# Optimization experiments

Measured on AMD Instinct MI355X. Metric: run time of the kernel, lower is better.

The kernel has to match this reference:

```python
import jax, jax.numpy as jnp
import numpy as np

B, L, U, G, H = 64, 110, 768, 512, 256
WP = WF = 10
NSP = 2
R = 2 * NSP * NSP      # 8 relation types
NB = 30                # RGCN num_bases
FF = 2048              # torch TransformerEncoderLayer default dim_feedforward
TAG = 7
N = B * L
NEG = -1e9


def _build_edges():
    # static windowed edge structure (all dialogues have length L)
    js, ks = [], []
    for j in range(L):
        for k in range(max(0, j - WP), min(L - 1, j + WF) + 1):
            js.append(j); ks.append(k)
    j = np.asarray(js, np.int32); k = np.asarray(ks, np.int32)
    c = (j >= k).astype(np.int32)  # edge_type suffix: '0' if j<k else '1'
    off = (np.arange(B, dtype=np.int32) * L)[:, None]
    src = (j[None, :] + off).reshape(-1)
    dst = (k[None, :] + off).reshape(-1)
    return src, dst, np.tile(k, B), np.tile(c, B)


def _ln(x, g, b):
    m = x.mean(-1, keepdims=True)
    v = ((x - m) ** 2).mean(-1, keepdims=True)
    return (x - m) / jnp.sqrt(v + 1e-5) * g + b


def _core(x, in_proj_w, in_proj_b, out_proj_w, out_proj_b, ln1_g, ln1_b,
          ff1_w, ff1_b, ff2_w, ff2_b, ln2_g, ln2_b, to_w, to_b, att_w,
          rgcn_basis, rgcn_comp, rgcn_root, rgcn_bias,
          gc_rel_w, gc_rel_b, gc_root_w, clf1_w, clf1_b, clf2_w, clf2_b,
          speaker, src, dst, k_local, cflag):
    # --- SeqContext: 1-layer, 1-head post-norm transformer (eval mode) ---
    qkv = x @ in_proj_w.T + in_proj_b
    q, kk, v = jnp.split(qkv, 3, axis=-1)
    attn = jax.nn.softmax(jnp.einsum('bqd,bkd->bqk', q, kk) / jnp.sqrt(jnp.float32(U)), -1)
    a = jnp.einsum('bqk,bkd->bqd', attn, v) @ out_proj_w.T + out_proj_b
    h = _ln(x + a, ln1_g, ln1_b)
    ff = jax.nn.relu(h @ ff1_w.T + ff1_b) @ ff2_w.T + ff2_b
    h = _ln(h + ff, ln2_g, ln2_b)
    feats = h @ to_w.T + to_b                      # (B, L, G) node features

    # --- EdgeAtt: windowed softmax attention, score[j,k] = x_j^T W x_k ---
    scores = jnp.einsum('bjd,de,bke->bjk', feats, att_w, feats)
    rel = jnp.arange(L)[None, :] - jnp.arange(L)[:, None]
    mask = (rel >= -WP) & (rel <= WF)
    alpha = jax.nn.softmax(jnp.where(mask[None], scores, NEG), -1)  # (B, L, L)

    xf = feats.reshape(N, G)
    edge_norm = alpha.reshape(N, L)[src, k_local]   # alpha[b, j, k] per edge

    # --- edge types from speakers: idx = (s1*NSP + s2)*2 + c ---
    sp = speaker.reshape(N)
    etype = (sp[src] * NSP + sp[dst]) * 2 + cflag

    # --- RGCNConv: basis decomposition, per-(node, relation) mean + root ---
    w_rel = jnp.einsum('rb,bgh->rgh', rgcn_comp, rgcn_basis)   # (R, G, H)
    xproj = jnp.einsum('ng,rgh->rnh', xf, w_rel)               # (R, N, H)
    msg = xproj[etype, src]                                    # (E, H)
    seg = dst * R + etype
    cnt = jax.ops.segment_sum(jnp.ones_like(edge_norm), seg, num_segments=N * R)
    msg = msg / jnp.maximum(cnt[seg], 1.0)[:, None]
    h1 = jax.ops.segment_sum(msg, dst, num_segments=N) + xf @ rgcn_root + rgcn_bias

    # --- GraphConv: sum-aggregate edge-weighted neighbors + root ---
    agg = jax.ops.segment_sum(edge_norm[:, None] * h1[src], dst, num_segments=N)
    h2 = agg @ gc_rel_w.T + gc_rel_b + h1 @ gc_root_w.T

    # --- Classifier (dropout inactive in eval) ---
    z = jnp.concatenate([xf, h2], axis=-1)
    return jax.nn.relu(z @ clf1_w.T + clf1_b) @ clf2_w.T + clf2_b  # (N, TAG)


def setup_inputs():
    key = jax.random.key(0)
    ks = jax.random.split(key, 16)
    def rn(i, shape, scale=0.02):
        return jax.random.normal(ks[i], shape, jnp.float32) * scale
    src, dst, k_local, cflag = _build_edges()
    return {
        'x': jax.random.normal(ks[0], (B, L, U), jnp.float32),
        'in_proj_w': rn(1, (3 * U, U)), 'in_proj_b': jnp.zeros((3 * U,), jnp.float32),
        'out_proj_w': rn(2, (U, U)), 'out_proj_b': jnp.zeros((U,), jnp.float32),
        'ln1_g': jnp.ones((U,), jnp.float32), 'ln1_b': jnp.zeros((U,), jnp.float32),
        'ff1_w': rn(3, (FF, U)), 'ff1_b': jnp.zeros((FF,), jnp.float32),
        'ff2_w': rn(4, (U, FF)), 'ff2_b': jnp.zeros((U,), jnp.float32),
        'ln2_g': jnp.ones((U,), jnp.float32), 'ln2_b': jnp.zeros((U,), jnp.float32),
        'to_w': rn(5, (G, U)), 'to_b': jnp.zeros((G,), jnp.float32),
        'att_w': rn(6, (G, G), 2.0 / (G + G)),
        'rgcn_basis': rn(7, (NB, G, H)), 'rgcn_comp': rn(8, (R, NB), 0.2),
        'rgcn_root': rn(9, (G, H)), 'rgcn_bias': jnp.zeros((H,), jnp.float32),
        'gc_rel_w': rn(10, (H, H)), 'gc_rel_b': jnp.zeros((H,), jnp.float32),
        'gc_root_w': rn(11, (H, H)),
        'clf1_w': rn(12, (H, G + H)), 'clf1_b': jnp.zeros((H,), jnp.float32),
        'clf2_w': rn(13, (TAG, H)), 'clf2_b': jnp.zeros((TAG,), jnp.float32),
        'speaker': jax.random.randint(ks[14], (B, L), 0, NSP, jnp.int32),
        'src': jnp.asarray(src), 'dst': jnp.asarray(dst),
        'k_local': jnp.asarray(k_local), 'cflag': jnp.asarray(cflag),
        'length': L,
    }


def reference(x, in_proj_w, in_proj_b, out_proj_w, out_proj_b, ln1_g, ln1_b,
              ff1_w, ff1_b, ff2_w, ff2_b, ln2_g, ln2_b, to_w, to_b, att_w,
              rgcn_basis, rgcn_comp, rgcn_root, rgcn_bias,
              gc_rel_w, gc_rel_b, gc_root_w, clf1_w, clf1_b, clf2_w, clf2_b,
              speaker, src, dst, k_local, cflag, length):
    return _core(x, in_proj_w, in_proj_b, out_proj_w, out_proj_b, ln1_g, ln1_b,
                 ff1_w, ff1_b, ff2_w, ff2_b, ln2_g, ln2_b, to_w, to_b, att_w,
                 rgcn_basis, rgcn_comp, rgcn_root, rgcn_bias,
                 gc_rel_w, gc_rel_b, gc_root_w, clf1_w, clf1_b, clf2_w, clf2_b,
                 speaker, src, dst, k_local, cflag)
```

## Files before the change

kernel.cpp:

```cpp
#include <hip/hip_runtime.h>
#include <hip/hip_bf16.h>
#include <math.h>

#define L_   110
#define B_   64
#define N_   7040
#define U_   768
#define G_   512
#define H_   256
#define FF_  2048
#define EPB_ 2200
#define NC_  2816

typedef __attribute__((ext_vector_type(4))) float f32x4;
typedef __attribute__((ext_vector_type(8))) short bf16x8;

__device__ __forceinline__ ushort f2b(float f) {
  union { __hip_bfloat16 h; ushort u; } cv;
  cv.h = __float2bfloat16(f);
  return cv.u;
}
__device__ __forceinline__ float b2f(ushort u) {
  union { float f; unsigned int i; } cv; cv.i = ((unsigned int)u) << 16; return cv.f;
}

__device__ __forceinline__ int edge_prefix(int j) {
  if (j <= 10)  return j * 11 + (j * (j - 1)) / 2;
  if (j <= 100) return 155 + (j - 10) * 21;
  return 2045 + ((141 - j) * (j - 100)) / 2;
}

struct PrepArgs {
  const float* cin[7]; ushort* cout[7]; int n4[7];
  const float* rb; const float* grel; const float* groot;
  const float* clf1w; const float* clf1bias; const float* grelb;
  const float* attw; const float* basis; const float* comp; const float* root;
  float* bias_comb; ushort* grelrootT; ushort* Wp; float* bias2; ushort* combw;
};

__global__ __launch_bounds__(256)
void prep_kernel(PrepArgs a)
{
  __shared__ float t[32][33];
  __shared__ float cs[240];
  const int y = blockIdx.y;
  const int tid = threadIdx.x;
  if (y < 7) {
    const int n4 = a.n4[y];
    const float* __restrict__ in = a.cin[y];
    ushort* __restrict__ out = a.cout[y];
    for (int i = blockIdx.x * 256 + tid; i < n4; i += gridDim.x * 256) {
      float4 v = ((const float4*)in)[i];
      ushort4 o;
      o.x = f2b(v.x); o.y = f2b(v.y); o.z = f2b(v.z); o.w = f2b(v.w);
      ((ushort4*)out)[i] = o;
    }
  } else if (y == 7) {
    const int total = NC_ + 65536 + 65536 + 131072 + 256;
    for (int i = blockIdx.x * 256 + tid; i < total; i += gridDim.x * 256) {
      if (i < NC_) {
        a.bias_comb[i] = (i < 2560) ? 0.f : a.rb[i - 2560];
      } else if (i < NC_ + 65536) {
        const int j = i - NC_;
        const int k = j >> 8, c = j & 255;
        a.grelrootT[(size_t)c * 256 + k] = f2b(a.grel[j]);
      } else if (i < NC_ + 131072) {
        const int j = i - NC_ - 65536;
        const int k = j >> 8, c = j & 255;
        a.grelrootT[(size_t)(256 + c) * 256 + k] = f2b(a.groot[j]);
      } else if (i < NC_ + 131072 + 131072) {
        const int j = i - NC_ - 131072;
        const int o = j >> 9, c = j & 511;
        a.Wp[(size_t)o * 1024 + c] = f2b(a.clf1w[(size_t)o * 768 + c]);
      } else {
        const int tt = i - (NC_ + 131072 + 131072);
        float s = a.clf1bias[tt];
        for (int k = 0; k < 256; ++k)
          s = fmaf(a.clf1w[(size_t)tt * 768 + 512 + k], a.grelb[k], s);
        a.bias2[tt] = s;
      }
    }
  } else {
    const int tx = tid & 31, ty = tid >> 5;
    if (blockIdx.x < 256) {
      const int r0 = (blockIdx.x >> 4) * 32, c0 = (blockIdx.x & 15) * 32;
      for (int i = ty; i < 32; i += 8)
        t[i][tx] = a.attw[(size_t)(r0 + i) * 512 + c0 + tx];
      __syncthreads();
      for (int i = ty; i < 32; i += 8)
        a.combw[(size_t)(c0 + i) * 512 + r0 + tx] = f2b(t[tx][i]);
    } else if (blockIdx.x < 384) {
      const int t2 = blockIdx.x - 256;
      const int g0 = (t2 & 15) * 32, h0 = (t2 >> 4) * 32;
      if (tid < 240) cs[tid] = a.comp[tid];
      for (int i = ty; i < 32; i += 8)
        t[i][tx] = a.root[(size_t)(g0 + i) * 256 + h0 + tx];
      __syncthreads();
      for (int i = ty; i < 32; i += 8)
        a.combw[(size_t)(2560 + h0 + i) * 512 + g0 + tx] = f2b(t[tx][i]);
      float acc[8][4] = {};
      for (int bb = 0; bb < 30; ++bb) {
        const float* bp = a.basis + (size_t)bb * (G_ * H_);
#pragma unroll
        for (int k = 0; k < 4; ++k) {
          float v = bp[(size_t)(g0 + ty + 8 * k) * 256 + h0 + tx];
#pragma unroll
          for (int r = 0; r < 8; ++r) acc[r][k] = fmaf(cs[r * 30 + bb], v, acc[r][k]);
        }
      }
      for (int r = 0; r < 8; ++r) {
        __syncthreads();
#pragma unroll
        for (int k = 0; k < 4; ++k) t[ty + 8 * k][tx] = acc[r][k];
        __syncthreads();
        for (int i = ty; i < 32; i += 8)
          a.combw[(size_t)(512 + r * 256 + h0 + i) * 512 + g0 + tx] = f2b(t[tx][i]);
      }
    }
  }
}

template<bool BIAS, bool RELU>
__global__ __launch_bounds__(256)
void mgemm_kernel(const ushort* __restrict__ A, const ushort* __restrict__ B,
                  const float* __restrict__ bias, ushort* __restrict__ Cb,
                  int K, int lda, int ldb, int ldc)
{
  __shared__ ushort sA[128 * 64];
  __shared__ ushort sB[128 * 64];
  const int tid = threadIdx.x;
  const int w = tid >> 6, l = tid & 63;

  const int gx = gridDim.x;
  const int nwg = gx * gridDim.y;
  const int lid = blockIdx.y * gx + blockIdx.x;
  const int q = nwg >> 3, r = nwg & 7;
  const int xcd = lid & 7, pos = lid >> 3;
  const int nlid = (xcd < r ? xcd * (q + 1) : r * (q + 1) + (xcd - r) * q) + pos;
  const int m0 = (nlid / gx) * 128, n0 = (nlid % gx) * 128;

  const int srow = l >> 3, sg = l & 7, rbase = w * 32;
  const int wr = w >> 1, wc = w & 1;
  const int lrow = l & 15, lk = l >> 4;
  const int xm = (l & 7) << 4;
  const int kb0 = (lk * 16) ^ xm;
  int aoff[4], boff[4];
#pragma unroll
  for (int i = 0; i < 4; ++i) {
    aoff[i] = (wr * 64 + i * 16 + lrow) * 128 + kb0;
    boff[i] = (wc * 64 + i * 16 + lrow) * 128 + kb0;
  }

  f32x4 acc[4][4];
#pragma unroll
  for (int i = 0; i < 4; ++i)
#pragma unroll
    for (int j = 0; j < 4; ++j) acc[i][j] = (f32x4){0.f, 0.f, 0.f, 0.f};

#define STAGE(k0)                                                              \
  {                                                                            \
    _Pragma("unroll")                                                          \
    for (int i = 0; i < 4; ++i) {                                              \
      const int trow = rbase + i * 8 + srow;                                   \
      const int koff = (sg * 8) ^ ((trow & 7) << 3);                           \
      const ushort* ga = A + (size_t)(m0 + trow) * lda + (k0) + koff;          \
      const ushort* gb = B + (size_t)(n0 + trow) * ldb + (k0) + koff;          \
      __builtin_amdgcn_global_load_lds(                                        \
          (const __attribute__((address_space(1))) void*)ga,                   \
          (__attribute__((address_space(3))) void*)&sA[(rbase + i * 8) * 64],  \
          16, 0, 0);                                                           \
      __builtin_amdgcn_global_load_lds(                                        \
          (const __attribute__((address_space(1))) void*)gb,                   \
          (__attribute__((address_space(3))) void*)&sB[(rbase + i * 8) * 64],  \
          16, 0, 0);                                                           \
    }                                                                          \
  }

  STAGE(0)
  for (int kt = 0;;) {
    __syncthreads();
#pragma unroll
    for (int h = 0; h < 2; ++h) {
      const int hx = h * 64;
      bf16x8 af[4], bfr[4];
#pragma unroll
      for (int i = 0; i < 4; ++i) {
        af[i]  = *(const bf16x8*)&sA[(aoff[i] ^ hx) >> 1];
        bfr[i] = *(const bf16x8*)&sB[(boff[i] ^ hx) >> 1];
      }
#pragma unroll
      for (int mi = 0; mi < 4; ++mi)
#pragma unroll
        for (int ni = 0; ni < 4; ++ni)
          acc[mi][ni] = __builtin_amdgcn_mfma_f32_16x16x32_bf16(
              af[mi], bfr[ni], acc[mi][ni], 0, 0, 0);
    }
    kt += 64;
    if (kt >= K) break;
    __syncthreads();
    STAGE(kt)
  }
#undef STAGE

  const int orow = m0 + wr * 64 + lk * 4;
  const int ocol = n0 + wc * 64 + lrow;
#pragma unroll
  for (int mi = 0; mi < 4; ++mi) {
#pragma unroll
    for (int r2 = 0; r2 < 4; ++r2) {
      const int row = orow + mi * 16 + r2;
#pragma unroll
      for (int ni = 0; ni < 4; ++ni) {
        const int col = ocol + ni * 16;
        float v = acc[mi][ni][r2];
        if constexpr (BIAS) v += bias[col];
        if constexpr (RELU) v = fmaxf(v, 0.f);
        Cb[(size_t)row * ldc + col] = f2b(v);
      }
    }
  }
}

template<bool BIAS, bool RELU>
__global__ __launch_bounds__(256)
void mgemm64_kernel(const ushort* __restrict__ A, const ushort* __restrict__ B,
                    const float* __restrict__ bias, ushort* __restrict__ Cb,
                    int K, int lda, int ldb, int ldc)
{
  __shared__ ushort sA[128 * 64];
  __shared__ ushort sB[64 * 64];
  const int tid = threadIdx.x;
  const int w = tid >> 6, l = tid & 63;

  const int gx = gridDim.x;
  const int nwg = gx * gridDim.y;
  const int lid = blockIdx.y * gx + blockIdx.x;
  const int q = nwg >> 3, r = nwg & 7;
  const int xcd = lid & 7, pos = lid >> 3;
  const int nlid = (xcd < r ? xcd * (q + 1) : r * (q + 1) + (xcd - r) * q) + pos;
  const int m0 = (nlid / gx) * 128, n0 = (nlid % gx) * 64;

  const int srow = l >> 3, sg = l & 7;
  const int lrow = l & 15, lk = l >> 4;
  const int xm = (l & 7) << 4;
  const int kb0 = (lk * 16) ^ xm;
  int aoff[2], boff[4];
#pragma unroll
  for (int i = 0; i < 2; ++i) aoff[i] = (w * 32 + i * 16 + lrow) * 128 + kb0;
#pragma unroll
  for (int i = 0; i < 4; ++i) boff[i] = (i * 16 + lrow) * 128 + kb0;

  f32x4 acc[2][4];
#pragma unroll
  for (int i = 0; i < 2; ++i)
#pragma unroll
    for (int j = 0; j < 4; ++j) acc[i][j] = (f32x4){0.f, 0.f, 0.f, 0.f};

#define STAGE64(k0)                                                            \
  {                                                                            \
    _Pragma("unroll")                                                          \
    for (int i = 0; i < 4; ++i) {                                              \
      const int trow = w * 32 + i * 8 + srow;                                  \
      const int koff = (sg * 8) ^ ((trow & 7) << 3);                           \
      const ushort* ga = A + (size_t)(m0 + trow) * lda + (k0) + koff;          \
      __builtin_amdgcn_global_load_lds(                                        \
          (const __attribute__((address_space(1))) void*)ga,                   \
          (__attribute__((address_space(3))) void*)&sA[(w * 32 + i * 8) * 64], \
          16, 0, 0);                                                           \
    }                                                                          \
    _Pragma("unroll")                                                          \
    for (int i = 0; i < 2; ++i) {                                              \
      const int trow = w * 16 + i * 8 + srow;                                  \
      const int koff = (sg * 8) ^ ((trow & 7) << 3);                           \
      const ushort* gb = B + (size_t)(n0 + trow) * ldb + (k0) + koff;          \
      __builtin_amdgcn_global_load_lds(                                        \
          (const __attribute__((address_space(1))) void*)gb,                   \
          (__attribute__((address_space(3))) void*)&sB[(w * 16 + i * 8) * 64], \
          16, 0, 0);                                                           \
    }                                                                          \
  }

  STAGE64(0)
  for (int kt = 0;;) {
    __syncthreads();
#pragma unroll
    for (int h = 0; h < 2; ++h) {
      const int hx = h * 64;
      bf16x8 af[2], bfr[4];
#pragma unroll
      for (int i = 0; i < 2; ++i) af[i] = *(const bf16x8*)&sA[(aoff[i] ^ hx) >> 1];
#pragma unroll
      for (int i = 0; i < 4; ++i) bfr[i] = *(const bf16x8*)&sB[(boff[i] ^ hx) >> 1];
#pragma unroll
      for (int mi = 0; mi < 2; ++mi)
#pragma unroll
        for (int ni = 0; ni < 4; ++ni)
          acc[mi][ni] = __builtin_amdgcn_mfma_f32_16x16x32_bf16(
              af[mi], bfr[ni], acc[mi][ni], 0, 0, 0);
    }
    kt += 64;
    if (kt >= K) break;
    __syncthreads();
    STAGE64(kt)
  }
#undef STAGE64

  const int orow = m0 + w * 32 + lk * 4;
  const int ocol = n0 + lrow;
#pragma unroll
  for (int mi = 0; mi < 2; ++mi) {
#pragma unroll
    for (int r2 = 0; r2 < 4; ++r2) {
      const int row = orow + mi * 16 + r2;
#pragma unroll
      for (int ni = 0; ni < 4; ++ni) {
        const int col = ocol + ni * 16;
        float v = acc[mi][ni][r2];
        if constexpr (BIAS) v += bias[col];
        if constexpr (RELU) v = fmaxf(v, 0.f);
        Cb[(size_t)row * ldc + col] = f2b(v);
      }
    }
  }
}

__global__ __launch_bounds__(256)
void vtrans_kernel(const ushort* __restrict__ qkvb, ushort* __restrict__ vt)
{
  __shared__ ushort t[32][34];
  const int b = blockIdx.z;
  const int r0 = blockIdx.y * 32;
  const int c0 = blockIdx.x * 32;
  const int tid = threadIdx.x;
  for (int e = tid; e < 512; e += 256) {
    const int ri = e >> 4, ci2 = (e & 15) * 2;
    ushort2 v = make_ushort2(0, 0);
    if (r0 + ri < L_)
      v = *(const ushort2*)&qkvb[((size_t)(b * L_) + r0 + ri) * 2304 + 1536 + c0 + ci2];
    t[ri][ci2] = v.x; t[ri][ci2 + 1] = v.y;
  }
  __syncthreads();
  for (int e = tid; e < 512; e += 256) {
    const int ci = e >> 4, ri2 = (e & 15) * 2;
    ushort2 o = make_ushort2(t[ri2][ci], t[ri2 + 1][ci]);
    *(ushort2*)&vt[((size_t)b * 768 + c0 + ci) * 128 + r0 + ri2] = o;
  }
}

__global__ __launch_bounds__(256)
void attnF_kernel(const ushort* __restrict__ qkvb, const ushort* __restrict__ vt,
                  const ushort* __restrict__ xb, const ushort* __restrict__ opw,
                  const float* __restrict__ opb, const float* __restrict__ g1,
                  const float* __restrict__ b1, ushort* __restrict__ hb)
{
  const int wg = blockIdx.x;
  const int xcd = wg & 7, slot = wg >> 3;
  const int b = xcd * 8 + slot / 7;
  const int qr0 = (slot % 7) * 16;
  const int tid = threadIdx.x, w = tid >> 6, l = tid & 63;
  __shared__ float  sS[16 * 128];
  __shared__ ushort sP[16 * 128];
  __shared__ ushort sC[16][776];
  __shared__ float  sRed[16][8];
  __shared__ float  sMean[16], sRstd[16];
  const int lrow = l & 15, lq = l >> 4;

  const ushort* Qbase = qkvb + ((size_t)(b * L_) + qr0 + lrow) * 2304 + lq * 8;
  f32x4 accS[2] = {{0.f,0.f,0.f,0.f},{0.f,0.f,0.f,0.f}};
  const int nf0 = w * 2;
  for (int k0 = 0; k0 < 768; k0 += 32) {
    bf16x8 aq = *(const bf16x8*)(Qbase + k0);
#pragma unroll
    for (int f = 0; f < 2; ++f) {
      const int nf = nf0 + f;
      if (nf < 7) {
        const ushort* Kp = qkvb + ((size_t)(b * L_) + nf * 16 + lrow) * 2304
                         + 768 + k0 + lq * 8;
        bf16x8 bk = *(const bf16x8*)Kp;
        accS[f] = __builtin_amdgcn_mfma_f32_16x16x32_bf16(aq, bk, accS[f], 0, 0, 0);
      }
    }
  }
  const float scale = 0.03608439182435161f;
#pragma unroll
  for (int f = 0; f < 2; ++f) {
    const int nf = nf0 + f;
    if (nf < 7) {
#pragma unroll
      for (int r = 0; r < 4; ++r)
        sS[(lq * 4 + r) * 128 + nf * 16 + lrow] = accS[f][r] * scale;
    }
  }
  __syncthreads();

  {
    const int row = w * 4 + lq;
    const int c0 = lrow;
    float m = -1e30f;
    for (int c = c0; c < L_; c += 16) m = fmaxf(m, sS[row * 128 + c]);
#pragma unroll
    for (int off = 8; off; off >>= 1) m = fmaxf(m, __shfl_xor(m, off));
    float pv[7];
    float sum = 0.f;
#pragma unroll
    for (int i = 0; i < 7; ++i) {
      const int c = c0 + i * 16;
      float e = (c < L_) ? __expf(sS[row * 128 + c] - m) : 0.f;
      pv[i] = e; sum += e;
    }
#pragma unroll
    for (int off = 8; off; off >>= 1) sum += __shfl_xor(sum, off);
    const float inv = 1.f / sum;
#pragma unroll
    for (int i = 0; i < 8; ++i) {
      const int c = c0 + i * 16;
      ushort pb = (i < 7 && c < L_) ? f2b(pv[i < 7 ? i : 0] * inv) : (ushort)0;
      const int g = (c >> 3) ^ (row & 7);
      sP[row * 128 + g * 8 + (c & 7)] = pb;
    }
  }
  __syncthreads();

  f32x4 accO[12];
#pragma unroll
  for (int i = 0; i < 12; ++i) accO[i] = (f32x4){0.f, 0.f, 0.f, 0.f};
#pragma unroll
  for (int ks = 0; ks < 4; ++ks) {
    const int k = ks * 32 + lq * 8;
    const int g = (k >> 3) ^ (lrow & 7);
    bf16x8 ap = *(const bf16x8*)&sP[lrow * 128 + g * 8];
#pragma unroll
    for (int i = 0; i < 12; ++i) {
      const int col = w * 192 + i * 16 + lrow;
      bf16x8 bv = *(const bf16x8*)(vt + ((size_t)b * 768 + col) * 128 + k);
      accO[i] = __builtin_amdgcn_mfma_f32_16x16x32_bf16(ap, bv, accO[i], 0, 0, 0);
    }
  }
#pragma unroll
  for (int i = 0; i < 12; ++i) {
    const int col = w * 192 + i * 16 + lrow;
#pragma unroll
    for (int r = 0; r < 4; ++r)
      sC[lq * 4 + r][col] = f2b(accO[i][r]);
  }
  __syncthreads();

  f32x4 acc2[12];
#pragma unroll
  for (int i = 0; i < 12; ++i) acc2[i] = (f32x4){0.f, 0.f, 0.f, 0.f};
  for (int k0 = 0; k0 < 768; k0 += 32) {
    bf16x8 af = *(const bf16x8*)&sC[lrow][k0 + lq * 8];
#pragma unroll
    for (int i = 0; i < 12; ++i) {
      const int col = w * 192 + i * 16 + lrow;
      bf16x8 bfr = *(const bf16x8*)(opw + (size_t)col * 768 + k0 + lq * 8);
      acc2[i] = __builtin_amdgcn_mfma_f32_16x16x32_bf16(af, bfr, acc2[i], 0, 0, 0);
    }
  }

  float vv[12][4];
  bool rv[4];
#pragma unroll
  for (int r = 0; r < 4; ++r) rv[r] = (qr0 + lq * 4 + r) < L_;
  float ssum[4] = {0.f, 0.f, 0.f, 0.f}, ssq[4] = {0.f, 0.f, 0.f, 0.f};
#pragma unroll
  for (int i = 0; i < 12; ++i) {
    const int col = w * 192 + i * 16 + lrow;
    const float bb = opb[col];
#pragma unroll
    for (int r = 0; r < 4; ++r) {
      float xv = 0.f;
      if (rv[r]) {
        const size_t grow = (size_t)(b * L_ + qr0 + lq * 4 + r);
        xv = b2f(xb[grow * 768 + col]);
      }
      float v = acc2[i][r] + bb + xv;
      vv[i][r] = v;
      ssum[r] += v; ssq[r] += v * v;
    }
  }
#pragma unroll
  for (int off = 1; off < 16; off <<= 1) {
#pragma unroll
    for (int r = 0; r < 4; ++r) {
      ssum[r] += __shfl_xor(ssum[r], off);
      ssq[r]  += __shfl_xor(ssq[r], off);
    }
  }
  if (lrow == 0) {
#pragma unroll
    for (int r = 0; r < 4; ++r) {
      sRed[lq * 4 + r][w] = ssum[r];
      sRed[lq * 4 + r][4 + w] = ssq[r];
    }
  }
  __syncthreads();
  if (tid < 16) {
    float S = sRed[tid][0] + sRed[tid][1] + sRed[tid][2] + sRed[tid][3];
    float Q = sRed[tid][4] + sRed[tid][5] + sRed[tid][6] + sRed[tid][7];
    float mn = S * (1.f / 768.f);
    float var = Q * (1.f / 768.f) - mn * mn;
    sMean[tid] = mn;
    sRstd[tid] = rsqrtf(var + 1e-5f);
  }
  __syncthreads();
#pragma unroll
  for (int i = 0; i < 12; ++i) {
    const int col = w * 192 + i * 16 + lrow;
    const float gg = g1[col], b2 = b1[col];
#pragma unroll
    for (int r = 0; r < 4; ++r) {
      if (rv[r]) {
        const int lr = lq * 4 + r;
        const size_t grow = (size_t)(b * L_ + qr0 + lr);
        hb[grow * 768 + col] = f2b((vv[i][r] - sMean[lr]) * sRstd[lr] * gg + b2);
      }
    }
  }
}

__global__ __launch_bounds__(256)
void ln_kernel(const ushort* __restrict__ Ab, const ushort* __restrict__ Bres,
               const float* __restrict__ g, const float* __restrict__ beta,
               ushort* __restrict__ outb)
{
  const int row = blockIdx.x, tid = threadIdx.x;
  const ushort* ap = Ab + (size_t)row * U_;
  const ushort* bp = Bres + (size_t)row * U_;
  float v0 = b2f(ap[tid])       + b2f(bp[tid]);
  float v1 = b2f(ap[tid + 256]) + b2f(bp[tid + 256]);
  float v2 = b2f(ap[tid + 512]) + b2f(bp[tid + 512]);
  float s = v0 + v1 + v2, sq = v0 * v0 + v1 * v1 + v2 * v2;
  __shared__ float red[8];
#pragma unroll
  for (int off = 32; off; off >>= 1) { s += __shfl_xor(s, off); sq += __shfl_xor(sq, off); }
  const int wave = tid >> 6, lane = tid & 63;
  if (lane == 0) { red[wave] = s; red[4 + wave] = sq; }
  __syncthreads();
  if (tid == 0) {
    float ts = red[0] + red[1] + red[2] + red[3];
    float tq = red[4] + red[5] + red[6] + red[7];
    float m = ts * (1.f / 768.f);
    float var = tq * (1.f / 768.f) - m * m;
    red[0] = m; red[1] = 1.f / sqrtf(var + 1e-5f);
  }
  __syncthreads();
  const float m = red[0], inv = red[1];
  ushort* ob = outb + (size_t)row * U_;
  ob[tid]       = f2b((v0 - m) * inv * g[tid]       + beta[tid]);
  ob[tid + 256] = f2b((v1 - m) * inv * g[tid + 256] + beta[tid + 256]);
  ob[tid + 512] = f2b((v2 - m) * inv * g[tid + 512] + beta[tid + 512]);
}

__global__ __launch_bounds__(256)
void graphfront_kernel(const ushort* __restrict__ combo, ushort* __restrict__ fcat2,
                       const int* __restrict__ speaker, float* __restrict__ edge_norm)
{
  const int tid = threadIdx.x;
  if (blockIdx.x < N_ / 8) {
    const int n = blockIdx.x * 8 + (tid >> 5);
    const int lane = tid & 31;
    const int b = n / L_, k = n - b * L_;
    const int j0 = max(0, k - 10), j1 = min(L_ - 1, k + 10);
    const int spk = speaker[n];
    float inv[4];
    {
      int cn[4] = {0, 0, 0, 0};
      for (int j = j0; j <= j1; ++j)
        cn[speaker[b * L_ + j] * 2 + (j >= k ? 1 : 0)]++;
#pragma unroll
      for (int q = 0; q < 4; ++q) inv[q] = cn[q] ? 1.f / (float)cn[q] : 0.f;
    }
    float acc[8] = {};
    for (int j = j0; j <= j1; ++j) {
      const int spj = speaker[b * L_ + j];
      const int c = (j >= k) ? 1 : 0;
      const int et = (spj * 2 + spk) * 2 + c;
      const float w = inv[spj * 2 + c];
      bf16x8 v = *(const bf16x8*)&combo[(size_t)(b * L_ + j) * NC_ + 512 + et * 256 + lane * 8];
#pragma unroll
      for (int i = 0; i < 8; ++i) acc[i] = fmaf(b2f((ushort)v[i]), w, acc[i]);
    }
    bf16x8 rt = *(const bf16x8*)&combo[(size_t)n * NC_ + 2560 + lane * 8];
    bf16x8 o;
#pragma unroll
    for (int i = 0; i < 8; ++i) o[i] = (short)f2b(acc[i] + b2f((ushort)rt[i]));
    *(bf16x8*)&fcat2[(size_t)n * 1024 + 768 + lane * 8] = o;
  } else {
    const int bj = blockIdx.x - N_ / 8;
    const int b = bj / L_, j = bj - b * L_;
    const int k0 = max(0, j - 10), k1 = min(L_ - 1, j + 10);
    __shared__ float s[32];
    const int wave = tid >> 6, lane = tid & 63;
    float tr[8];
    {
      bf16x8 tv = *(const bf16x8*)&combo[(size_t)bj * NC_ + lane * 8];
#pragma unroll
      for (int i = 0; i < 8; ++i) tr[i] = b2f((ushort)tv[i]);
    }
    for (int k = k0 + wave; k <= k1; k += 4) {
      bf16x8 v = *(const bf16x8*)&fcat2[(size_t)(b * L_ + k) * 1024 + lane * 8];
      float sc = 0.f;
#pragma unroll
      for (int i = 0; i < 8; ++i) sc = fmaf(b2f((ushort)v[i]), tr[i], sc);
#pragma unroll
      for (int off = 32; off; off >>= 1) sc += __shfl_xor(sc, off);
      if (lane == 0) s[k - k0] = sc;
    }
    __syncthreads();
    if (tid == 0) {
      const int W = k1 - k0 + 1;
      float m = -1e30f;
      for (int t = 0; t < W; ++t) m = fmaxf(m, s[t]);
      float sum = 0.f;
      for (int t = 0; t < W; ++t) { float e = __expf(s[t] - m); s[t] = e; sum += e; }
      const float inv = 1.f / sum;
      const int base = b * EPB_ + edge_prefix(j);
      for (int t = 0; t < W; ++t) edge_norm[base + t] = s[t] * inv;
    }
  }
}

__global__ __launch_bounds__(256)
void gcn_gather2_kernel(const float* __restrict__ edge_norm,
                        ushort* __restrict__ fcat2)
{
  const int tid = threadIdx.x;
  const int n = blockIdx.x * 8 + (tid >> 5);
  const int lane = tid & 31;
  const int b = n / L_, k = n - b * L_;
  const int j0 = max(0, k - 10), j1 = min(L_ - 1, k + 10);
  float acc[8] = {};
  for (int j = j0; j <= j1; ++j) {
    const float w = edge_norm[b * EPB_ + edge_prefix(j) + (k - max(0, j - 10))];
    bf16x8 v = *(const bf16x8*)&fcat2[(size_t)(b * L_ + j) * 1024 + 768 + lane * 8];
#pragma unroll
    for (int i = 0; i < 8; ++i) acc[i] = fmaf(b2f((ushort)v[i]), w, acc[i]);
  }
  bf16x8 o;
#pragma unroll
  for (int i = 0; i < 8; ++i) o[i] = (short)f2b(acc[i]);
  *(bf16x8*)&fcat2[(size_t)n * 1024 + 512 + lane * 8] = o;
}

__global__ __launch_bounds__(256)
void clf2_kernel(const ushort* __restrict__ hid, const float* __restrict__ w,
                 const float* __restrict__ bias, float* __restrict__ out)
{
  __shared__ float wsm[7 * H_];
  const int tid = threadIdx.x;
  for (int i = tid; i < 7 * H_; i += 256) wsm[i] = w[i];
  __syncthreads();
  const int idx = blockIdx.x * 256 + threadIdx.x;
  if (idx < N_ * 7) {
    const int n = idx / 7, t = idx - n * 7;
    const ushort* hp = hid + (size_t)n * H_;
    const float* wp = wsm + t * H_;
    float acc = bias[t];
    for (int d0 = 0; d0 < H_; d0 += 8) {
      bf16x8 v = *(const bf16x8*)(hp + d0);
#pragma unroll
      for (int i = 0; i < 8; ++i) acc = fmaf(b2f((ushort)v[i]), wp[d0 + i], acc);
    }
    out[idx] = acc;
  }
}

extern "C" void kernel_launch(void* const* d_in, const int* in_sizes, int n_in,
                              void* d_out, int out_size, void* d_ws, size_t ws_size,
                              hipStream_t stream)
{
  const float* x          = (const float*)d_in[0];
  const float* in_proj_w  = (const float*)d_in[1];
  const float* in_proj_b  = (const float*)d_in[2];
  const float* out_proj_w = (const float*)d_in[3];
  const float* out_proj_b = (const float*)d_in[4];
  const float* ln1_g      = (const float*)d_in[5];
  const float* ln1_b      = (const float*)d_in[6];
  const float* ff1_w      = (const float*)d_in[7];
  const float* ff1_b      = (const float*)d_in[8];
  const float* ff2_w      = (const float*)d_in[9];
  const float* ff2_b      = (const float*)d_in[10];
  const float* ln2_g      = (const float*)d_in[11];
  const float* ln2_b      = (const float*)d_in[12];
  const float* to_w       = (const float*)d_in[13];
  const float* to_b       = (const float*)d_in[14];
  const float* att_w      = (const float*)d_in[15];
  const float* rgcn_basis = (const float*)d_in[16];
  const float* rgcn_comp  = (const float*)d_in[17];
  const float* rgcn_root  = (const float*)d_in[18];
  const float* rgcn_bias  = (const float*)d_in[19];
  const float* gc_rel_w   = (const float*)d_in[20];
  const float* gc_rel_b   = (const float*)d_in[21];
  const float* gc_root_w  = (const float*)d_in[22];
  const float* clf1_w     = (const float*)d_in[23];
  const float* clf1_b     = (const float*)d_in[24];
  const float* clf2_w     = (const float*)d_in[25];
  const float* clf2_b     = (const float*)d_in[26];
  const int*   speaker    = (const int*)d_in[27];
  float* out = (float*)d_out;
  char* p = (char*)d_ws;

  ushort* R1b    = (ushort*)p;
  p += (size_t)N_ * 2304 * 4;
  ushort* ffoB   = (ushort*)p;
  float*  en     = (float*)(p + (size_t)N_ * 512 * 4);
  p += (size_t)N_ * 768 * 4;
  ushort* vt    = (ushort*)p;
  ushort* hidB  = (ushort*)p;
  p += (size_t)N_ * 768 * 4;
  ushort* xb    = (ushort*)p;
  p += (size_t)N_ * 768 * 2;
  ushort* hb    = (ushort*)p;
  p += (size_t)N_ * 768 * 2;
  ushort* fcat2 = (ushort*)p;
  p += (size_t)N_ * 1024 * 2;
  ushort* in_projb = (ushort*)p; p += (size_t)2304 * 768 * 2;
  ushort* out_projb= (ushort*)p; p += (size_t)768 * 768 * 2;
  ushort* ff1b     = (ushort*)p; p += (size_t)2048 * 768 * 2;
  ushort* ff2b     = (ushort*)p; p += (size_t)768 * 2048 * 2;
  ushort* tob      = (ushort*)p; p += (size_t)512 * 768 * 2;
  ushort* combw    = (ushort*)p; p += (size_t)NC_ * 512 * 2;
  ushort* clf1b16  = (ushort*)p; p += (size_t)256 * 768 * 2;
  ushort* Wp       = (ushort*)p; p += (size_t)256 * 1024 * 2;
  ushort* grelrootT= (ushort*)p; p += (size_t)512 * 256 * 2;
  float*  bias_comb= (float*)p;  p += NC_ * 4;
  float*  bias2    = (float*)p;  p += 256 * 4;

  PrepArgs pa;
  pa.cin[0] = x;          pa.cout[0] = xb;        pa.n4[0] = N_ * 768 / 4;
  pa.cin[1] = in_proj_w;  pa.cout[1] = in_projb;  pa.n4[1] = 2304 * 768 / 4;
  pa.cin[2] = out_proj_w; pa.cout[2] = out_projb; pa.n4[2] = 768 * 768 / 4;
  pa.cin[3] = ff1_w;      pa.cout[3] = ff1b;      pa.n4[3] = 2048 * 768 / 4;
  pa.cin[4] = ff2_w;      pa.cout[4] = ff2b;      pa.n4[4] = 768 * 2048 / 4;
  pa.cin[5] = to_w;       pa.cout[5] = tob;       pa.n4[5] = 512 * 768 / 4;
  pa.cin[6] = clf1_w;     pa.cout[6] = clf1b16;   pa.n4[6] = 256 * 768 / 4;
  pa.rb = rgcn_bias; pa.grel = gc_rel_w; pa.groot = gc_root_w;
  pa.clf1w = clf1_w; pa.clf1bias = clf1_b; pa.grelb = gc_rel_b;
  pa.attw = att_w; pa.basis = rgcn_basis; pa.comp = rgcn_comp; pa.root = rgcn_root;
  pa.bias_comb = bias_comb; pa.grelrootT = grelrootT; pa.Wp = Wp;
  pa.bias2 = bias2; pa.combw = combw;
  prep_kernel<<<dim3(768, 9), 256, 0, stream>>>(pa);
  mgemm64_kernel<false, false><<<dim3(8, 2), 256, 0, stream>>>(
      clf1b16 + 512, grelrootT, nullptr, Wp + 512, 256, 768, 256, 1024);

  mgemm_kernel<true, false><<<dim3(18, 55), 256, 0, stream>>>(
      xb, in_projb, in_proj_b, R1b, 768, 768, 768, 2304);
  vtrans_kernel<<<dim3(24, 4, 64), 256, 0, stream>>>(R1b, vt);
  attnF_kernel<<<448, 256, 0, stream>>>(R1b, vt, xb, out_projb, out_proj_b,
                                        ln1_g, ln1_b, hb);
  mgemm_kernel<true, true><<<dim3(16, 55), 256, 0, stream>>>(
      hb, ff1b, ff1_b, R1b, 768, 768, 768, 2048);
  mgemm64_kernel<true, false><<<dim3(12, 55), 256, 0, stream>>>(
      R1b, ff2b, ff2_b, ffoB, 2048, 2048, 2048, 768);
  ln_kernel<<<N_, 256, 0, stream>>>(hb, ffoB, ln2_g, ln2_b, hb);
  mgemm64_kernel<true, false><<<dim3(8, 55), 256, 0, stream>>>(
      hb, tob, to_b, fcat2, 768, 768, 768, 1024);
  mgemm_kernel<true, false><<<dim3(22, 55), 256, 0, stream>>>(
      fcat2, combw, bias_comb, R1b, 512, 1024, 512, NC_);
  graphfront_kernel<<<N_ / 8 + N_, 256, 0, stream>>>(R1b, fcat2, speaker, en);
  gcn_gather2_kernel<<<N_ / 8, 256, 0, stream>>>(en, fcat2);
  mgemm64_kernel<true, true><<<dim3(4, 55), 256, 0, stream>>>(
      fcat2, Wp, bias2, hidB, 1024, 1024, 1024, 256);
  clf2_kernel<<<(N_ * 7 + 255) / 256, 256, 0, stream>>>(hidB, clf2_w, clf2_b, out);
}
```

Before: 354.7 us.

## Split fused attention+out-proj+LayerNorm kernel into attention, tiled GEMM, and LN

The fused attention kernel used to compute the context, then the 768x768 output projection, then the residual LayerNorm, all inside each 16-row block. That projection streamed the whole out_proj weight from global memory once per 16-row tile. Now the attention kernel only writes the context to a buffer. The projection runs as a separate tiled GEMM (mgemm64) that reuses weights better, and the existing ln_kernel applies the residual and LayerNorm. This adds an extra global round trip for the context and projection output, plus two more kernel launches.

```diff
diff --git a/kernel.cpp b/kernel.cpp
--- a/kernel.cpp
+++ b/kernel.cpp
@@ -348,10 +348,8 @@
 }
 
 __global__ __launch_bounds__(256)
-void attnF_kernel(const ushort* __restrict__ qkvb, const ushort* __restrict__ vt,
-                  const ushort* __restrict__ xb, const ushort* __restrict__ opw,
-                  const float* __restrict__ opb, const float* __restrict__ g1,
-                  const float* __restrict__ b1, ushort* __restrict__ hb)
+void attnM_kernel(const ushort* __restrict__ qkvb, const ushort* __restrict__ vt,
+                  ushort* __restrict__ ctxb)
 {
   const int wg = blockIdx.x;
   const int xcd = wg & 7, slot = wg >> 3;
@@ -360,9 +358,6 @@
   const int tid = threadIdx.x, w = tid >> 6, l = tid & 63;
   __shared__ float  sS[16 * 128];
   __shared__ ushort sP[16 * 128];
-  __shared__ ushort sC[16][776];
-  __shared__ float  sRed[16][8];
-  __shared__ float  sMean[16], sRstd[16];
   const int lrow = l & 15, lq = l >> 4;
 
   const ushort* Qbase = qkvb + ((size_t)(b * L_) + qr0 + lrow) * 2304 + lq * 8;
@@ -440,81 +435,10 @@
   for (int i = 0; i < 12; ++i) {
     const int col = w * 192 + i * 16 + lrow;
 #pragma unroll
-    for (int r = 0; r < 4; ++r)
-      sC[lq * 4 + r][col] = f2b(accO[i][r]);
-  }
-  __syncthreads();
-
-  f32x4 acc2[12];
-#pragma unroll
-  for (int i = 0; i < 12; ++i) acc2[i] = (f32x4){0.f, 0.f, 0.f, 0.f};
-  for (int k0 = 0; k0 < 768; k0 += 32) {
-    bf16x8 af = *(const bf16x8*)&sC[lrow][k0 + lq * 8];
-#pragma unroll
-    for (int i = 0; i < 12; ++i) {
-      const int col = w * 192 + i * 16 + lrow;
-      bf16x8 bfr = *(const bf16x8*)(opw + (size_t)col * 768 + k0 + lq * 8);
-      acc2[i] = __builtin_amdgcn_mfma_f32_16x16x32_bf16(af, bfr, acc2[i], 0, 0, 0);
-    }
-  }
-
-  float vv[12][4];
-  bool rv[4];
-#pragma unroll
-  for (int r = 0; r < 4; ++r) rv[r] = (qr0 + lq * 4 + r) < L_;
-  float ssum[4] = {0.f, 0.f, 0.f, 0.f}, ssq[4] = {0.f, 0.f, 0.f, 0.f};
-#pragma unroll
-  for (int i = 0; i < 12; ++i) {
-    const int col = w * 192 + i * 16 + lrow;
-    const float bb = opb[col];
-#pragma unroll
     for (int r = 0; r < 4; ++r) {
-      float xv = 0.f;
-      if (rv[r]) {
-        const size_t grow = (size_t)(b * L_ + qr0 + lq * 4 + r);
-        xv = b2f(xb[grow * 768 + col]);
-      }
-      float v = acc2[i][r] + bb + xv;
-      vv[i][r] = v;
-      ssum[r] += v; ssq[r] += v * v;
-    }
-  }
-#pragma unroll
-  for (int off = 1; off < 16; off <<= 1) {
-#pragma unroll
-    for (int r = 0; r < 4; ++r) {
-      ssum[r] += __shfl_xor(ssum[r], off);
-      ssq[r]  += __shfl_xor(ssq[r], off);
-    }
-  }
-  if (lrow == 0) {
-#pragma unroll
-    for (int r = 0; r < 4; ++r) {
-      sRed[lq * 4 + r][w] = ssum[r];
-      sRed[lq * 4 + r][4 + w] = ssq[r];
-    }
-  }
-  __syncthreads();
-  if (tid < 16) {
-    float S = sRed[tid][0] + sRed[tid][1] + sRed[tid][2] + sRed[tid][3];
-    float Q = sRed[tid][4] + sRed[tid][5] + sRed[tid][6] + sRed[tid][7];
-    float mn = S * (1.f / 768.f);
-    float var = Q * (1.f / 768.f) - mn * mn;
-    sMean[tid] = mn;
-    sRstd[tid] = rsqrtf(var + 1e-5f);
-  }
-  __syncthreads();
-#pragma unroll
-  for (int i = 0; i < 12; ++i) {
-    const int col = w * 192 + i * 16 + lrow;
-    const float gg = g1[col], b2 = b1[col];
-#pragma unroll
-    for (int r = 0; r < 4; ++r) {
-      if (rv[r]) {
-        const int lr = lq * 4 + r;
-        const size_t grow = (size_t)(b * L_ + qr0 + lr);
-        hb[grow * 768 + col] = f2b((vv[i][r] - sMean[lr]) * sRstd[lr] * gg + b2);
-      }
+      const int row = qr0 + lq * 4 + r;
+      if (row < L_)
+        ctxb[((size_t)b * L_ + row) * 768 + col] = f2b(accO[i][r]);
     }
   }
 }
@@ -703,7 +627,8 @@
 
   ushort* R1b    = (ushort*)p;
   p += (size_t)N_ * 2304 * 4;
-  ushort* ffoB   = (ushort*)p;
+  ushort* aprojB = (ushort*)p;
+  ushort* ffoB   = aprojB;
   float*  en     = (float*)(p + (size_t)N_ * 512 * 4);
   p += (size_t)N_ * 768 * 4;
   ushort* vt    = (ushort*)p;
@@ -714,6 +639,7 @@
   ushort* hb    = (ushort*)p;
   p += (size_t)N_ * 768 * 2;
   ushort* fcat2 = (ushort*)p;
+  ushort* ctxb  = (ushort*)p;
   p += (size_t)N_ * 1024 * 2;
   ushort* in_projb = (ushort*)p; p += (size_t)2304 * 768 * 2;
   ushort* out_projb= (ushort*)p; p += (size_t)768 * 768 * 2;
@@ -747,8 +673,10 @@
   mgemm_kernel<true, false><<<dim3(18, 55), 256, 0, stream>>>(
       xb, in_projb, in_proj_b, R1b, 768, 768, 768, 2304);
   vtrans_kernel<<<dim3(24, 4, 64), 256, 0, stream>>>(R1b, vt);
-  attnF_kernel<<<448, 256, 0, stream>>>(R1b, vt, xb, out_projb, out_proj_b,
-                                        ln1_g, ln1_b, hb);
+  attnM_kernel<<<448, 256, 0, stream>>>(R1b, vt, ctxb);
+  mgemm64_kernel<true, false><<<dim3(12, 55), 256, 0, stream>>>(
+      ctxb, out_projb, out_proj_b, aprojB, 768, 768, 768, 768);
+  ln_kernel<<<N_, 256, 0, stream>>>(xb, aprojB, ln1_g, ln1_b, hb);
   mgemm_kernel<true, true><<<dim3(16, 55), 256, 0, stream>>>(
       hb, ff1b, ff1_b, R1b, 768, 768, 768, 2048);
   mgemm64_kernel<true, false><<<dim3(12, 55), 256, 0, stream>>>(
```

New measurement: 302.5 us. 14.7% less time.
